# Optimization experiments

Hardware: AMD Instinct MI355X
Metric: run time of the kernel (lower is better)

## Reference

```python
import jax, jax.numpy as jnp
import numpy as np

EPS = 1e-5  # BatchNorm eps (PyTorch default)


def gcn_conv(x, edge_index, W, b):
    """PyG GCNConv with add_self_loops=True, normalize=True.
    out[j] = sum_{(i->j)} x_w[i] / sqrt(deg_i * deg_j) + x_w[j] / deg_j + b,
    deg_j = 1 + in-degree(j) (self-loop included)."""
    n = x.shape[0]
    src, dst = edge_index[0], edge_index[1]
    ones = jnp.ones(src.shape[0], x.dtype)
    deg = 1.0 + jax.ops.segment_sum(ones, dst, num_segments=n)  # [n]
    dis = jax.lax.rsqrt(deg)
    xw = x @ W  # [n, out]
    msg = xw[src] * (dis[src] * dis[dst])[:, None]  # gather + per-edge norm
    agg = jax.ops.segment_sum(msg, dst, num_segments=n)  # scatter-add
    agg = agg + xw * (1.0 / deg)[:, None]  # self-loop term
    return agg + b


def bn_relu(x, gamma, beta):
    # BatchNorm1d over the node dim (training-mode batch stats) + ReLU
    mean = x.mean(axis=0)
    var = x.var(axis=0)
    return jax.nn.relu((x - mean) * jax.lax.rsqrt(var + EPS) * gamma + beta)


def wireframe_gnn(x, edge_index, layers, fcW, fcb):
    feats = [x]
    h = x
    for (W, b, g, be) in layers:  # fixed small n_layers loop
        h = bn_relu(gcn_conv(h, edge_index, W, b), g, be)
        feats.append(h)
    cat = jnp.concatenate(feats, axis=1)
    return jax.nn.relu(cat @ fcW + fcb)


N_L, N_J = 50000, 25000
D_FC, NF = 1024, 256
E_L, E_J = 400000, 100000
L_LAB, J_LAB = 10, 3


def setup_inputs() -> dict:
    key = jax.random.key(0)
    ks = iter(jax.random.split(key, 48))
    p = lambda shape: (jax.random.normal(next(ks), shape, jnp.float32) * 0.02)
    inp = {}
    inp["line_features"] = jax.random.normal(next(ks), (N_L, D_FC), jnp.float32)
    inp["junction_features"] = jax.random.normal(next(ks), (N_J, NF), jnp.float32)
    inp["line_edge_index"] = jax.random.randint(next(ks), (2, E_L), 0, N_L, jnp.int64)
    inp["junction_edge_index"] = jax.random.randint(next(ks), (2, E_J), 0, N_J, jnp.int64)
    # line GNN: 1024 -> 512 -> 256, concat 1792 -> fc 1024
    inp["lg_W1"], inp["lg_b1"] = p((D_FC, D_FC // 2)), p((D_FC // 2,))
    inp["lg_g1"], inp["lg_be1"] = jnp.ones(D_FC // 2, jnp.float32), jnp.zeros(D_FC // 2, jnp.float32)
    inp["lg_W2"], inp["lg_b2"] = p((D_FC // 2, D_FC // 4)), p((D_FC // 4,))
    inp["lg_g2"], inp["lg_be2"] = jnp.ones(D_FC // 4, jnp.float32), jnp.zeros(D_FC // 4, jnp.float32)
    cat_l = D_FC + D_FC // 2 + D_FC // 4  # 1792
    inp["lg_fcW"], inp["lg_fcb"] = p((cat_l, D_FC)), p((D_FC,))
    # fc_lines: 1024 -> 1024 -> 1024 -> L_LAB (dim_loi*n_pts1 == dim_fc == 1024)
    inp["fl_W1"], inp["fl_b1"] = p((D_FC, D_FC)), p((D_FC,))
    inp["fl_W2"], inp["fl_b2"] = p((D_FC, D_FC)), p((D_FC,))
    inp["fl_W3"], inp["fl_b3"] = p((D_FC, L_LAB)), p((L_LAB,))
    # junction GNN: 256 -> 128 -> 64, concat 448 -> fc 256
    inp["jg_W1"], inp["jg_b1"] = p((NF, NF // 2)), p((NF // 2,))
    inp["jg_g1"], inp["jg_be1"] = jnp.ones(NF // 2, jnp.float32), jnp.zeros(NF // 2, jnp.float32)
    inp["jg_W2"], inp["jg_b2"] = p((NF // 2, NF // 4)), p((NF // 4,))
    inp["jg_g2"], inp["jg_be2"] = jnp.ones(NF // 4, jnp.float32), jnp.zeros(NF // 4, jnp.float32)
    cat_j = NF + NF // 2 + NF // 4  # 448
    inp["jg_fcW"], inp["jg_fcb"] = p((cat_j, NF)), p((NF,))
    # fc_junction: 256 -> 64 -> J_LAB
    m = NF // 4
    inp["fj_W1"], inp["fj_b1"] = p((NF, m)), p((m,))
    inp["fj_W2"], inp["fj_b2"] = p((m, J_LAB)), p((J_LAB,))
    return inp


def reference(line_features, junction_features, line_edge_index, junction_edge_index,
              lg_W1, lg_b1, lg_g1, lg_be1, lg_W2, lg_b2, lg_g2, lg_be2, lg_fcW, lg_fcb,
              fl_W1, fl_b1, fl_W2, fl_b2, fl_W3, fl_b3,
              jg_W1, jg_b1, jg_g1, jg_be1, jg_W2, jg_b2, jg_g2, jg_be2, jg_fcW, jg_fcb,
              fj_W1, fj_b1, fj_W2, fj_b2):
    # line branch
    h = wireframe_gnn(line_features, line_edge_index,
                      [(lg_W1, lg_b1, lg_g1, lg_be1), (lg_W2, lg_b2, lg_g2, lg_be2)],
                      lg_fcW, lg_fcb)
    h = jax.nn.relu(h @ fl_W1 + fl_b1)
    h = jax.nn.relu(h @ fl_W2 + fl_b2)
    line_logits = h @ fl_W3 + fl_b3
    # junction branch
    g = wireframe_gnn(junction_features, junction_edge_index,
                      [(jg_W1, jg_b1, jg_g1, jg_be1), (jg_W2, jg_b2, jg_g2, jg_be2)],
                      jg_fcW, jg_fcb)
    g = jax.nn.relu(g @ fj_W1 + fj_b1)
    junction_logits = g @ fj_W2 + fj_b2
    return (line_logits, junction_logits)
```

## Files before the change

### kernel.cpp

```cpp
#include <hip/hip_runtime.h>
#include <stdint.h>
#include <stddef.h>

typedef _Float16 f16;
typedef _Float16 f16x8 __attribute__((ext_vector_type(8)));
typedef _Float16 f16x4_t __attribute__((ext_vector_type(4)));
typedef float floatx4 __attribute__((ext_vector_type(4)));

template <int N> struct F16Vec { typedef f16 type __attribute__((ext_vector_type(N))); };

#define BN_EPS 1e-5f

struct WtJob { const float* W; f16* Wt; int K; int N; int tN; int tilebase; };
struct WtBatch { WtJob j[12]; int njobs; int ntiles; };

__global__ void k_wt_tiled(WtBatch b) {
  __shared__ float T[32][33];
  int bt = blockIdx.x;
  int i = 0;
  #pragma unroll 1
  while (i + 1 < b.njobs && bt >= b.j[i + 1].tilebase) ++i;
  WtJob J = b.j[i];
  int t = bt - J.tilebase;
  int tr = t / J.tN, tc = t - tr * J.tN;
  int ty = threadIdx.x >> 5, tx = threadIdx.x & 31;
  #pragma unroll
  for (int s = 0; s < 32; s += 8) {
    int k = tr * 32 + ty + s, n = tc * 32 + tx;
    if (k < J.K && n < J.N) T[ty + s][tx] = J.W[(size_t)k * J.N + n];
  }
  __syncthreads();
  #pragma unroll
  for (int s = 0; s < 32; s += 8) {
    int n = tc * 32 + ty + s, k = tr * 32 + tx;
    if (n < J.N && k < J.K) J.Wt[(size_t)n * J.K + k] = (f16)T[tx][ty + s];
  }
}

__global__ void k_cvt_cols(const float* __restrict__ src, f16* __restrict__ dst,
                           int n, int c, int ldd, int coff) {
  int t = blockIdx.x * blockDim.x + threadIdx.x;
  int cq = c >> 2;
  if (t >= n * cq) return;
  int r = t / cq, j = (t - r * cq) << 2;
  float4 v = *(const float4*)(src + (size_t)r * c + j);
  f16x4_t o; o[0] = (f16)v.x; o[1] = (f16)v.y; o[2] = (f16)v.z; o[3] = (f16)v.w;
  *(f16x4_t*)(dst + (size_t)r * ldd + coff + j) = o;
}

__global__ void k_count2(const int* __restrict__ dL, int EL, int* __restrict__ cntL,
                         const int* __restrict__ dJ, int EJ, int* __restrict__ cntJ) {
  int t = blockIdx.x * blockDim.x + threadIdx.x;
  if (t < EL) atomicAdd(&cntL[dL[t]], 1);
  else if (t < EL + EJ) atomicAdd(&cntJ[dJ[t - EL]], 1);
}

__global__ void k_scan4(const int* __restrict__ cnt, int n, int* __restrict__ rowstart,
                        float* __restrict__ dis) {
  __shared__ int wsum[16];
  __shared__ int carry_s;
  int tid = threadIdx.x, lane = tid & 63, wv = tid >> 6;
  if (tid == 0) { carry_s = 0; rowstart[0] = 0; }
  __syncthreads();
  for (int base = 0; base < n; base += 4096) {
    int i4 = base + tid * 4;
    int4 c = {0, 0, 0, 0};
    if (i4 < n) c = *(const int4*)(cnt + i4);
    int s0 = c.x, s1 = s0 + c.y, s2 = s1 + c.z, s3 = s2 + c.w;
    int x = s3;
    #pragma unroll
    for (int off = 1; off < 64; off <<= 1) {
      int y = __shfl_up(x, off, 64);
      if (lane >= off) x += y;
    }
    if (lane == 63) wsum[wv] = x;
    __syncthreads();
    if (wv == 0) {
      int s = (lane < 16) ? wsum[lane] : 0;
      #pragma unroll
      for (int off = 1; off < 16; off <<= 1) {
        int y = __shfl_up(s, off, 64);
        if (lane >= off) s += y;
      }
      if (lane < 16) wsum[lane] = s;
    }
    __syncthreads();
    int waveoff = (wv == 0) ? 0 : wsum[wv - 1];
    int excl = (x - s3) + waveoff + carry_s;
    if (i4 < n) {
      rowstart[i4 + 1] = excl + s0;
      rowstart[i4 + 2] = excl + s1;
      rowstart[i4 + 3] = excl + s2;
      rowstart[i4 + 4] = excl + s3;
      dis[i4 + 0] = rsqrtf(1.0f + (float)c.x);
      dis[i4 + 1] = rsqrtf(1.0f + (float)c.y);
      dis[i4 + 2] = rsqrtf(1.0f + (float)c.z);
      dis[i4 + 3] = rsqrtf(1.0f + (float)c.w);
    }
    __syncthreads();
    if (tid == 1023) carry_s = excl + s3;
    __syncthreads();
  }
}

__global__ void k_fill2(const int* __restrict__ eiL, int EL, const int* __restrict__ rsL,
                        int* __restrict__ fillL, int* __restrict__ cixL,
                        const int* __restrict__ eiJ, int EJ, const int* __restrict__ rsJ,
                        int* __restrict__ fillJ, int* __restrict__ cixJ) {
  int t = blockIdx.x * blockDim.x + threadIdx.x;
  if (t < EL) {
    int s = eiL[t], d = eiL[EL + t];
    int pos = atomicAdd(&fillL[d], 1);
    cixL[rsL[d] + pos] = s;
  } else if (t < EL + EJ) {
    int u = t - EL;
    int s = eiJ[u], d = eiJ[EJ + u];
    int pos = atomicAdd(&fillJ[d], 1);
    cixJ[rsJ[d] + pos] = s;
  }
}

template <int CPL>
__global__ void k_gather_f16(const f16* __restrict__ xw, int C,
                             const int* __restrict__ rowstart, const int* __restrict__ colidx,
                             const float* __restrict__ dis, const float* __restrict__ bias,
                             f16* __restrict__ dst, int ldd, int coff, int n) {
  typedef typename F16Vec<CPL>::type V;
  int w = threadIdx.x >> 6, l = threadIdx.x & 63;
  int j = blockIdx.x * 4 + w;
  if (j >= n) return;
  float dj = dis[j];
  int rs = rowstart[j], re = rowstart[j + 1];
  int c0 = l * CPL;
  float acc[CPL];
  {
    V p = *(const V*)(xw + (size_t)j * C + c0);
    float s = dj * dj;
    #pragma unroll
    for (int t = 0; t < CPL; ++t) acc[t] = (float)p[t] * s;
  }
  int e = rs;
  for (; e + 2 <= re; e += 2) {
    int s0 = colidx[e], s1 = colidx[e + 1];
    float f0 = dis[s0] * dj, f1 = dis[s1] * dj;
    V p0 = *(const V*)(xw + (size_t)s0 * C + c0);
    V p1 = *(const V*)(xw + (size_t)s1 * C + c0);
    #pragma unroll
    for (int t = 0; t < CPL; ++t) acc[t] += (float)p0[t] * f0 + (float)p1[t] * f1;
  }
  if (e < re) {
    int s0 = colidx[e];
    float f0 = dis[s0] * dj;
    V p0 = *(const V*)(xw + (size_t)s0 * C + c0);
    #pragma unroll
    for (int t = 0; t < CPL; ++t) acc[t] += (float)p0[t] * f0;
  }
  V o;
  #pragma unroll
  for (int t = 0; t < CPL; ++t) o[t] = (f16)(acc[t] + bias[c0 + t]);
  *(V*)(dst + (size_t)j * ldd + coff + c0) = o;
}

__global__ void k_stats(const f16* __restrict__ v, int ldd, int coff, int n, int C,
                        float* __restrict__ sum, float* __restrict__ sumsq) {
  int c = blockIdx.x * blockDim.x + threadIdx.x;
  if (c >= C) return;
  int r0 = blockIdx.y * 128, r1 = min(r0 + 128, n);
  float s = 0.f, s2 = 0.f;
  for (int r = r0; r < r1; ++r) {
    float x = (float)v[(size_t)r * ldd + coff + c];
    s += x; s2 += x * x;
  }
  atomicAdd(&sum[c], s);
  atomicAdd(&sumsq[c], s2);
}

__global__ void k_bnparam(const float* __restrict__ sum, const float* __restrict__ sumsq,
                          const float* __restrict__ gamma, const float* __restrict__ beta,
                          int n, int C, float* __restrict__ scale, float* __restrict__ shift) {
  int c = blockIdx.x * blockDim.x + threadIdx.x;
  if (c >= C) return;
  float mean = sum[c] / (float)n;
  float var = sumsq[c] / (float)n - mean * mean;
  float sc = gamma[c] * rsqrtf(var + BN_EPS);
  scale[c] = sc;
  shift[c] = beta[c] - mean * sc;
}

__global__ void k_bnapply_ip(f16* __restrict__ v, int ldd, int coff, int n, int C,
                             const float* __restrict__ scale, const float* __restrict__ shift) {
  int t = blockIdx.x * blockDim.x + threadIdx.x;
  int cq = C >> 2;
  if (t >= n * cq) return;
  int r = t / cq, c = (t - r * cq) << 2;
  f16* p = v + (size_t)r * ldd + coff + c;
  f16x4_t x = *(f16x4_t*)p;
  float4 sc = *(const float4*)(scale + c);
  float4 sh = *(const float4*)(shift + c);
  f16x4_t o;
  o[0] = (f16)fmaxf((float)x[0] * sc.x + sh.x, 0.f);
  o[1] = (f16)fmaxf((float)x[1] * sc.y + sh.y, 0.f);
  o[2] = (f16)fmaxf((float)x[2] * sc.z + sh.z, 0.f);
  o[3] = (f16)fmaxf((float)x[3] * sc.w + sh.w, 0.f);
  *(f16x4_t*)p = o;
}

__global__ __launch_bounds__(256)
void k_gemm(const f16* __restrict__ A, int lda,
            const f16* __restrict__ Bt,
            void* __restrict__ Cv, int ldc,
            const float* __restrict__ bias, int relu, int outf,
            int M, int N, int K, int mt, int nt, int per) {
  __shared__ f16 Ash[2][128 * 32];
  __shared__ f16 Bsh[2][128 * 32];
  int b = blockIdx.x;
  int g = (b & 7) * per + (b >> 3);
  if (g >= mt * nt) return;
  int tm = (g / nt) * 128, tn = (g % nt) * 128;
  int tid = threadIdx.x, l = tid & 63, w = tid >> 6;

  const f16* ag[2]; const f16* bg[2];
  uint32_t lof[2];
  #pragma unroll
  for (int j = 0; j < 2; ++j) {
    int rl = w * 32 + j * 16 + (l >> 2);
    int ck = l & 3;
    int lc = ck ^ ((rl >> 1) & 3);
    int gr = tm + rl; if (gr > M - 1) gr = M - 1;
    int gn = tn + rl; if (gn > N - 1) gn = N - 1;
    ag[j] = A + (size_t)gr * lda + lc * 8;
    bg[j] = Bt + (size_t)gn * K + lc * 8;
    lof[j] = (uint32_t)(w * 32 + j * 16) * 64;
  }

  int wm = (w >> 1) * 64, wn = (w & 1) * 64;
  int q = l >> 4, l15 = l & 15;
  uint32_t aoffb[4], boffb[4];
  #pragma unroll
  for (int i = 0; i < 4; ++i) {
    int m = wm + i * 16 + l15;
    int n2 = wn + i * 16 + l15;
    aoffb[i] = (uint32_t)(m * 32 + (q ^ ((m >> 1) & 3)) * 8) * 2;
    boffb[i] = (uint32_t)(n2 * 32 + (q ^ ((n2 >> 1) & 3)) * 8) * 2;
  }

  floatx4 acc[4][4];
  #pragma unroll
  for (int i = 0; i < 4; ++i)
    #pragma unroll
    for (int j = 0; j < 4; ++j) acc[i][j] = (floatx4){0.f, 0.f, 0.f, 0.f};

  int nk = K >> 5;
  #pragma unroll
  for (int j = 0; j < 2; ++j) {
    __builtin_amdgcn_global_load_lds(
        (const __attribute__((address_space(1))) void*)ag[j],
        (__attribute__((address_space(3))) void*)((char*)Ash + lof[j]), 16, 0, 0);
    __builtin_amdgcn_global_load_lds(
        (const __attribute__((address_space(1))) void*)bg[j],
        (__attribute__((address_space(3))) void*)((char*)Bsh + lof[j]), 16, 0, 0);
    ag[j] += 32; bg[j] += 32;
  }

  for (int i = 0; i < nk; ++i) {
    __syncthreads();
    if (i + 1 < nk) {
      uint32_t d = ((i + 1) & 1) ? 8192u : 0u;
      #pragma unroll
      for (int j = 0; j < 2; ++j) {
        __builtin_amdgcn_global_load_lds(
            (const __attribute__((address_space(1))) void*)ag[j],
            (__attribute__((address_space(3))) void*)((char*)Ash + d + lof[j]), 16, 0, 0);
        __builtin_amdgcn_global_load_lds(
            (const __attribute__((address_space(1))) void*)bg[j],
            (__attribute__((address_space(3))) void*)((char*)Bsh + d + lof[j]), 16, 0, 0);
        ag[j] += 32; bg[j] += 32;
      }
    }
    uint32_t s = (i & 1) ? 8192u : 0u;
    f16x8 af[4], bf[4];
    #pragma unroll
    for (int ii = 0; ii < 4; ++ii) {
      af[ii] = *(const f16x8*)((const char*)Ash + s + aoffb[ii]);
      bf[ii] = *(const f16x8*)((const char*)Bsh + s + boffb[ii]);
    }
    #pragma unroll
    for (int mi = 0; mi < 4; ++mi)
      #pragma unroll
      for (int ni = 0; ni < 4; ++ni)
        acc[mi][ni] = __builtin_amdgcn_mfma_f32_16x16x32_f16(af[mi], bf[ni], acc[mi][ni], 0, 0, 0);
  }

  #pragma unroll
  for (int ni = 0; ni < 4; ++ni) {
    int col = tn + wn + ni * 16 + l15;
    if (col >= N) continue;
    float bv = bias ? bias[col] : 0.f;
    #pragma unroll
    for (int mi = 0; mi < 4; ++mi) {
      int rowb = tm + wm + mi * 16 + q * 4;
      #pragma unroll
      for (int r = 0; r < 4; ++r) {
        int row = rowb + r;
        if (row < M) {
          float v = acc[mi][ni][r] + bv;
          if (relu) v = fmaxf(v, 0.f);
          if (outf) ((float*)Cv)[(size_t)row * ldc + col] = v;
          else      ((f16*)Cv)[(size_t)row * ldc + col] = (f16)v;
        }
      }
    }
  }
}

#define G_BAR()   __builtin_amdgcn_s_barrier()
#define G_LGKM0() asm volatile("s_waitcnt lgkmcnt(0)" ::: "memory")

#define MFMA_PHASE(NI, B0v, B1v)                                              \
  __builtin_amdgcn_s_setprio(1);                                              \
  _Pragma("unroll")                                                           \
  for (int mi = 0; mi < 8; ++mi) {                                            \
    acc[mi][NI] = __builtin_amdgcn_mfma_f32_16x16x32_f16(B0v, af[mi][0], acc[mi][NI], 0, 0, 0); \
    acc[mi][NI] = __builtin_amdgcn_mfma_f32_16x16x32_f16(B1v, af[mi][1], acc[mi][NI], 0, 0, 0); \
  }                                                                           \
  __builtin_amdgcn_s_setprio(0);

__global__ __launch_bounds__(512, 2)
void k_gemm256(const f16* __restrict__ A, int lda,
               const f16* __restrict__ Bt,
               f16* __restrict__ C, int ldc,
               const float* __restrict__ bias, int relu,
               int M, int N, int K, int mt, int nt) {
  __shared__ char lds[131072];
  char* ldsc = (char*)lds;
  int nwg = mt * nt;
  int b = blockIdx.x;
  int xcd = b & 7, lid = b >> 3;
  int q8 = nwg >> 3, r8 = nwg & 7;
  int wg = (xcd < r8 ? xcd * (q8 + 1) : r8 * (q8 + 1) + (xcd - r8) * q8) + lid;
  int tm = (wg / nt) * 256, tn = (wg % nt) * 256;
  int tid = threadIdx.x, l = tid & 63, w = tid >> 6;
  int wm = w >> 2, wn = w & 3;
  int q = l >> 4, l15 = l & 15;
  int nk = K >> 6;

  int r0 = tid >> 3, r1 = r0 + 64;
  int ck = (tid & 7) ^ (r0 & 7);
  int gmA0a = tm + r0;        if (gmA0a > M - 1) gmA0a = M - 1;
  int gmA0b = tm + r1;        if (gmA0b > M - 1) gmA0b = M - 1;
  int gmA1a = tm + 128 + r0;  if (gmA1a > M - 1) gmA1a = M - 1;
  int gmA1b = tm + 128 + r1;  if (gmA1b > M - 1) gmA1b = M - 1;
  int gnB0a = tn + r0;        if (gnB0a > N - 1) gnB0a = N - 1;
  int gnB0b = tn + r1;        if (gnB0b > N - 1) gnB0b = N - 1;
  int gnB1a = tn + 128 + r0;  if (gnB1a > N - 1) gnB1a = N - 1;
  int gnB1b = tn + 128 + r1;  if (gnB1b > N - 1) gnB1b = N - 1;
  const f16* pA0a = A + (size_t)gmA0a * lda + ck * 8;
  const f16* pA0b = A + (size_t)gmA0b * lda + ck * 8;
  const f16* pA1a = A + (size_t)gmA1a * lda + ck * 8;
  const f16* pA1b = A + (size_t)gmA1b * lda + ck * 8;
  const f16* pB0a = Bt + (size_t)gnB0a * K + ck * 8;
  const f16* pB0b = Bt + (size_t)gnB0b * K + ck * 8;
  const f16* pB1a = Bt + (size_t)gnB1a * K + ck * 8;
  const f16* pB1b = Bt + (size_t)gnB1b * K + ck * 8;
  uint32_t dst0 = (uint32_t)tid * 16;

  auto ST2 = [&](const f16*& pa, const f16*& pb, uint32_t dst) {
    __builtin_amdgcn_global_load_lds(
        (const __attribute__((address_space(1))) void*)pa,
        (__attribute__((address_space(3))) void*)(ldsc + dst), 16, 0, 0);
    __builtin_amdgcn_global_load_lds(
        (const __attribute__((address_space(1))) void*)pb,
        (__attribute__((address_space(3))) void*)(ldsc + dst + 8192), 16, 0, 0);
    pa += 64; pb += 64;
  };
  auto SA0 = [&](uint32_t bb) { ST2(pA0a, pA0b, bb + dst0); };
  auto SA1 = [&](uint32_t bb) { ST2(pA1a, pA1b, bb + 16384u + dst0); };
  auto SB0 = [&](uint32_t bb) { ST2(pB0a, pB0b, bb + 32768u + dst0); };
  auto SB1 = [&](uint32_t bb) { ST2(pB1a, pB1b, bb + 49152u + dst0); };

  uint32_t abase = (uint32_t)((wm * 128 + l15) * 128);
  uint32_t bbase = (uint32_t)(32768 + (wn * 64 + l15) * 128);
  uint32_t cof0 = (uint32_t)(((0 + q) ^ (l15 & 7)) * 16);
  uint32_t cof1 = (uint32_t)(((4 + q) ^ (l15 & 7)) * 16);

  floatx4 acc[8][4];
  #pragma unroll
  for (int i = 0; i < 8; ++i)
    #pragma unroll
    for (int j = 0; j < 4; ++j) acc[i][j] = (floatx4){0.f, 0.f, 0.f, 0.f};

  SA0(0u); SA1(0u); SB0(0u); SB1(0u);
  if (nk > 1) { SA0(65536u); SA1(65536u); SB0(65536u); }
  asm volatile("s_waitcnt vmcnt(6)" ::: "memory");
  G_BAR();

  f16x8 af[8][2];
  for (int t = 0; t < nk; ++t) {
    uint32_t cb = (t & 1) ? 65536u : 0u;
    uint32_t ob = 65536u - cb;
    const char* cbp = ldsc + cb;
    if (t + 1 < nk) SB1(ob);
    #pragma unroll
    for (int mi = 0; mi < 8; ++mi) {
      af[mi][0] = *(const f16x8*)(cbp + abase + mi * 2048 + cof0);
      af[mi][1] = *(const f16x8*)(cbp + abase + mi * 2048 + cof1);
    }
    f16x8 b00 = *(const f16x8*)(cbp + bbase + cof0);
    f16x8 b01 = *(const f16x8*)(cbp + bbase + cof1);
    G_BAR(); G_LGKM0();
    MFMA_PHASE(0, b00, b01);
    G_BAR();
    if (t + 2 < nk) SA0(cb);
    f16x8 b10 = *(const f16x8*)(cbp + bbase + 2048 + cof0);
    f16x8 b11 = *(const f16x8*)(cbp + bbase + 2048 + cof1);
    G_BAR(); G_LGKM0();
    MFMA_PHASE(1, b10, b11);
    G_BAR();
    if (t + 2 < nk) SA1(cb);
    f16x8 b20 = *(const f16x8*)(cbp + bbase + 4096 + cof0);
    f16x8 b21 = *(const f16x8*)(cbp + bbase + 4096 + cof1);
    f16x8 b30 = *(const f16x8*)(cbp + bbase + 6144 + cof0);
    f16x8 b31 = *(const f16x8*)(cbp + bbase + 6144 + cof1);
    G_BAR(); G_LGKM0();
    MFMA_PHASE(2, b20, b21);
    G_BAR();
    if (t + 2 < nk) {
      SB0(cb);
      asm volatile("s_waitcnt vmcnt(6)" ::: "memory");
    } else {
      asm volatile("s_waitcnt vmcnt(0)" ::: "memory");
    }
    G_BAR();
    MFMA_PHASE(3, b30, b31);
  }

  #pragma unroll
  for (int mi = 0; mi < 8; ++mi) {
    int m = tm + wm * 128 + mi * 16 + l15;
    if (m >= M) continue;
    f16* crow = C + (size_t)m * ldc;
    #pragma unroll
    for (int ni = 0; ni < 4; ++ni) {
      int n0 = tn + wn * 64 + ni * 16 + q * 4;
      floatx4 v = acc[mi][ni];
      if (bias) {
        float4 bv = *(const float4*)(bias + n0);
        v[0] += bv.x; v[1] += bv.y; v[2] += bv.z; v[3] += bv.w;
      }
      if (relu) {
        v[0] = fmaxf(v[0], 0.f); v[1] = fmaxf(v[1], 0.f);
        v[2] = fmaxf(v[2], 0.f); v[3] = fmaxf(v[3], 0.f);
      }
      f16x4_t o;
      o[0] = (f16)v[0]; o[1] = (f16)v[1]; o[2] = (f16)v[2]; o[3] = (f16)v[3];
      *(f16x4_t*)(crow + n0) = o;
    }
  }
}

extern "C" void kernel_launch(void* const* d_in, const int* in_sizes, int n_in,
                              void* d_out, int out_size, void* d_ws, size_t ws_size,
                              hipStream_t stream) {
  (void)in_sizes; (void)n_in; (void)out_size; (void)ws_size;
  const int NL = 50000, NJ = 25000, EL = 400000, EJ = 100000;

  const float* x_l  = (const float*)d_in[0];
  const float* x_j  = (const float*)d_in[1];
  const int*   ei_l = (const int*)d_in[2];
  const int*   ei_j = (const int*)d_in[3];
  const float* lgW1 = (const float*)d_in[4];  const float* lgb1 = (const float*)d_in[5];
  const float* lgg1 = (const float*)d_in[6];  const float* lgbe1= (const float*)d_in[7];
  const float* lgW2 = (const float*)d_in[8];  const float* lgb2 = (const float*)d_in[9];
  const float* lgg2 = (const float*)d_in[10]; const float* lgbe2= (const float*)d_in[11];
  const float* lgfcW= (const float*)d_in[12]; const float* lgfcb= (const float*)d_in[13];
  const float* flW1 = (const float*)d_in[14]; const float* flb1 = (const float*)d_in[15];
  const float* flW2 = (const float*)d_in[16]; const float* flb2 = (const float*)d_in[17];
  const float* flW3 = (const float*)d_in[18]; const float* flb3 = (const float*)d_in[19];
  const float* jgW1 = (const float*)d_in[20]; const float* jgb1 = (const float*)d_in[21];
  const float* jgg1 = (const float*)d_in[22]; const float* jgbe1= (const float*)d_in[23];
  const float* jgW2 = (const float*)d_in[24]; const float* jgb2 = (const float*)d_in[25];
  const float* jgg2 = (const float*)d_in[26]; const float* jgbe2= (const float*)d_in[27];
  const float* jgfcW= (const float*)d_in[28]; const float* jgfcb= (const float*)d_in[29];
  const float* fjW1 = (const float*)d_in[30]; const float* fjb1 = (const float*)d_in[31];
  const float* fjW2 = (const float*)d_in[32]; const float* fjb2 = (const float*)d_in[33];

  char* ws = (char*)d_ws;
  size_t off = 0;
  auto alloc = [&](size_t bytes) -> char* {
    char* p = ws + off;
    off += (bytes + 255) & ~(size_t)255;
    return p;
  };

  f16* cat16 = (f16*)alloc((size_t)NL * 1792 * 2);
  f16* hA    = (f16*)alloc((size_t)NL * 1024 * 2);
  f16* hB    = (f16*)alloc((size_t)NL * 1024 * 2);
  f16*  xw16  = (f16*)hB;
  f16* catJ  = (f16*)alloc((size_t)NJ * 448 * 2);
  f16* hJA   = (f16*)alloc((size_t)NJ * 256 * 2);
  f16* hJB   = (f16*)alloc((size_t)NJ * 64 * 2);
  f16*  xwJ   = (f16*)hB;

  f16* W1t   = (f16*)alloc((size_t)1024 * 512 * 2);
  f16* W2t   = (f16*)alloc((size_t)512 * 256 * 2);
  f16* fcWt  = (f16*)alloc((size_t)1792 * 1024 * 2);
  f16* flW1t = (f16*)alloc((size_t)1024 * 1024 * 2);
  f16* flW2t = (f16*)alloc((size_t)1024 * 1024 * 2);
  f16* flW3t = (f16*)alloc((size_t)1024 * 16 * 2);
  f16* jW1t  = (f16*)alloc((size_t)256 * 128 * 2);
  f16* jW2t  = (f16*)alloc((size_t)128 * 64 * 2);
  f16* jfcWt = (f16*)alloc((size_t)448 * 256 * 2);
  f16* fjW1t = (f16*)alloc((size_t)256 * 64 * 2);
  f16* fjW2t = (f16*)alloc((size_t)64 * 4 * 2);

  int* zero0 = (int*)alloc(((size_t)2 * NL + 2 * NJ + 1920) * 4);
  int* cntL  = zero0;
  int* fillL = cntL + NL;
  int* cntJ  = fillL + NL;
  int* fillJ = cntJ + NJ;
  float* stats = (float*)(fillJ + NJ);
  float* sum1L = stats;        float* sq1L = stats + 512;
  float* sum2L = stats + 1024; float* sq2L = stats + 1280;
  float* sum1J = stats + 1536; float* sq1J = stats + 1664;
  float* sum2J = stats + 1792; float* sq2J = stats + 1856;

  int* rsL   = (int*)alloc((size_t)(NL + 4) * 4);
  int* cixL  = (int*)alloc((size_t)EL * 4);
  float* disL= (float*)alloc((size_t)NL * 4);
  int* rsJ   = (int*)alloc((size_t)(NJ + 4) * 4);
  int* cixJ  = (int*)alloc((size_t)EJ * 4);
  float* disJ= (float*)alloc((size_t)NJ * 4);
  float* scalc = (float*)alloc(512 * 4);
  float* shftc = (float*)alloc(512 * 4);

  auto cdiv = [](int a, int b) { return (a + b - 1) / b; };

  auto gemm = [&](const f16* A, int lda, const f16* Bt, void* Cc, int ldc,
                  const float* bias, int relu, int outf, int M, int N, int K) {
    if (!outf && (N & 255) == 0 && N >= 256 && (K & 63) == 0 && K >= 128) {
      int mt = cdiv(M, 256), nt = N >> 8;
      k_gemm256<<<mt * nt, 512, 0, stream>>>(A, lda, Bt, (f16*)Cc, ldc, bias, relu,
                                             M, N, K, mt, nt);
    } else {
      int mt = cdiv(M, 128), nt = cdiv(N, 128);
      int per = cdiv(mt * nt, 8);
      k_gemm<<<8 * per, 256, 0, stream>>>(A, lda, Bt, Cc, ldc, bias, relu, outf,
                                          M, N, K, mt, nt, per);
    }
  };
  auto bn = [&](f16* v, int ldd, int coff, int n, int C,
                float* sum, float* sumsq, const float* gamma, const float* beta) {
    dim3 gs(cdiv(C, 256), cdiv(n, 128));
    k_stats<<<gs, 256, 0, stream>>>(v, ldd, coff, n, C, sum, sumsq);
    k_bnparam<<<cdiv(C, 256), 256, 0, stream>>>(sum, sumsq, gamma, beta, n, C, scalc, shftc);
    k_bnapply_ip<<<cdiv(n * (C >> 2), 256), 256, 0, stream>>>(v, ldd, coff, n, C, scalc, shftc);
  };

  hipMemsetAsync(zero0, 0, ((size_t)2 * NL + 2 * NJ + 1920) * 4, stream);

  {
    WtBatch B2; int base = 0, nj = 0;
    auto add = [&](const float* W, f16* Wt, int K, int N) {
      int tK = cdiv(K, 32), tN = cdiv(N, 32);
      B2.j[nj++] = WtJob{W, Wt, K, N, tN, base};
      base += tK * tN;
    };
    add(lgW1, W1t, 1024, 512);
    add(lgW2, W2t, 512, 256);
    add(lgfcW, fcWt, 1792, 1024);
    add(flW1, flW1t, 1024, 1024);
    add(flW2, flW2t, 1024, 1024);
    add(flW3, flW3t, 1024, 10);
    add(jgW1, jW1t, 256, 128);
    add(jgW2, jW2t, 128, 64);
    add(jgfcW, jfcWt, 448, 256);
    add(fjW1, fjW1t, 256, 64);
    add(fjW2, fjW2t, 64, 3);
    B2.njobs = nj; B2.ntiles = base;
    k_wt_tiled<<<base, 256, 0, stream>>>(B2);
  }

  k_cvt_cols<<<cdiv(NL * 256, 256), 256, 0, stream>>>(x_l, cat16, NL, 1024, 1792, 0);
  k_cvt_cols<<<cdiv(NJ * 64, 256), 256, 0, stream>>>(x_j, catJ, NJ, 256, 448, 0);

  k_count2<<<cdiv(EL + EJ, 256), 256, 0, stream>>>(ei_l + EL, EL, cntL, ei_j + EJ, EJ, cntJ);
  k_scan4<<<1, 1024, 0, stream>>>(cntL, NL, rsL, disL);
  k_scan4<<<1, 1024, 0, stream>>>(cntJ, NJ, rsJ, disJ);
  k_fill2<<<cdiv(EL + EJ, 256), 256, 0, stream>>>(ei_l, EL, rsL, fillL, cixL,
                                                  ei_j, EJ, rsJ, fillJ, cixJ);

  gemm(cat16, 1792, W1t, xw16, 512, nullptr, 0, 0, NL, 512, 1024);
  k_gather_f16<8><<<cdiv(NL, 4), 256, 0, stream>>>(xw16, 512, rsL, cixL, disL, lgb1,
                                                   cat16, 1792, 1024, NL);
  bn(cat16, 1792, 1024, NL, 512, sum1L, sq1L, lgg1, lgbe1);

  gemm(cat16 + 1024, 1792, W2t, xw16, 256, nullptr, 0, 0, NL, 256, 512);
  k_gather_f16<4><<<cdiv(NL, 4), 256, 0, stream>>>(xw16, 256, rsL, cixL, disL, lgb2,
                                                   cat16, 1792, 1536, NL);
  bn(cat16, 1792, 1536, NL, 256, sum2L, sq2L, lgg2, lgbe2);

  gemm(cat16, 1792, fcWt, hA, 1024, lgfcb, 1, 0, NL, 1024, 1792);
  gemm(hA, 1024, flW1t, hB, 1024, flb1, 1, 0, NL, 1024, 1024);
  gemm(hB, 1024, flW2t, hA, 1024, flb2, 1, 0, NL, 1024, 1024);
  gemm(hA, 1024, flW3t, (float*)d_out, 10, flb3, 0, 1, NL, 10, 1024);

  gemm(catJ, 448, jW1t, xwJ, 128, nullptr, 0, 0, NJ, 128, 256);
  k_gather_f16<2><<<cdiv(NJ, 4), 256, 0, stream>>>(xwJ, 128, rsJ, cixJ, disJ, jgb1,
                                                   catJ, 448, 256, NJ);
  bn(catJ, 448, 256, NJ, 128, sum1J, sq1J, jgg1, jgbe1);

  gemm(catJ + 256, 448, jW2t, xwJ, 64, nullptr, 0, 0, NJ, 64, 128);
  k_gather_f16<1><<<cdiv(NJ, 4), 256, 0, stream>>>(xwJ, 64, rsJ, cixJ, disJ, jgb2,
                                                   catJ, 448, 384, NJ);
  bn(catJ, 448, 384, NJ, 64, sum2J, sq2J, jgg2, jgbe2);

  gemm(catJ, 448, jfcWt, hJA, 256, jgfcb, 1, 0, NJ, 256, 448);
  gemm(hJA, 256, fjW1t, hJB, 64, fjb1, 1, 0, NJ, 64, 256);
  gemm(hJB, 64, fjW2t, (float*)d_out + (size_t)NL * 10, 3, fjb2, 0, 1, NJ, 3, 64);
}
```

Before: 1.507 ms.

## Restructure 256x256 GEMM main loop to stream A fragments per M-pair

```diff
diff --git a/kernel.cpp b/kernel.cpp
--- a/kernel.cpp
+++ b/kernel.cpp
@@ -313,15 +313,30 @@
   }
 }
 
-#define G_BAR()   __builtin_amdgcn_s_barrier()
+#define G_BAR()   asm volatile("s_barrier" ::: "memory")
 #define G_LGKM0() asm volatile("s_waitcnt lgkmcnt(0)" ::: "memory")
 
-#define MFMA_PHASE(NI, B0v, B1v)                                              \
+#define READ_BF_ALL()                                                         \
+  _Pragma("unroll")                                                           \
+  for (int ni = 0; ni < 4; ++ni) {                                            \
+    bf[ni][0] = *(const f16x8*)(cbp + bbase + ni * 2048 + cof0);              \
+    bf[ni][1] = *(const f16x8*)(cbp + bbase + ni * 2048 + cof1);              \
+  }
+
+#define READ_AFP(P)                                                           \
+  afp[0][0] = *(const f16x8*)(cbp + abase + (2 * (P)) * 2048 + cof0);         \
+  afp[0][1] = *(const f16x8*)(cbp + abase + (2 * (P)) * 2048 + cof1);         \
+  afp[1][0] = *(const f16x8*)(cbp + abase + (2 * (P) + 1) * 2048 + cof0);     \
+  afp[1][1] = *(const f16x8*)(cbp + abase + (2 * (P) + 1) * 2048 + cof1);
+
+#define MFMA_PAIR(P)                                                          \
   __builtin_amdgcn_s_setprio(1);                                              \
   _Pragma("unroll")                                                           \
-  for (int mi = 0; mi < 8; ++mi) {                                            \
-    acc[mi][NI] = __builtin_amdgcn_mfma_f32_16x16x32_f16(B0v, af[mi][0], acc[mi][NI], 0, 0, 0); \
-    acc[mi][NI] = __builtin_amdgcn_mfma_f32_16x16x32_f16(B1v, af[mi][1], acc[mi][NI], 0, 0, 0); \
+  for (int ni = 0; ni < 4; ++ni) {                                            \
+    acc[2*(P)][ni]   = __builtin_amdgcn_mfma_f32_16x16x32_f16(bf[ni][0], afp[0][0], acc[2*(P)][ni], 0, 0, 0);   \
+    acc[2*(P)][ni]   = __builtin_amdgcn_mfma_f32_16x16x32_f16(bf[ni][1], afp[0][1], acc[2*(P)][ni], 0, 0, 0);   \
+    acc[2*(P)+1][ni] = __builtin_amdgcn_mfma_f32_16x16x32_f16(bf[ni][0], afp[1][0], acc[2*(P)+1][ni], 0, 0, 0); \
+    acc[2*(P)+1][ni] = __builtin_amdgcn_mfma_f32_16x16x32_f16(bf[ni][1], afp[1][1], acc[2*(P)+1][ni], 0, 0, 0); \
   }                                                                           \
   __builtin_amdgcn_s_setprio(0);
 
@@ -390,48 +405,36 @@
     for (int j = 0; j < 4; ++j) acc[i][j] = (floatx4){0.f, 0.f, 0.f, 0.f};
 
   SA0(0u); SA1(0u); SB0(0u); SB1(0u);
-  if (nk > 1) { SA0(65536u); SA1(65536u); SB0(65536u); }
-  asm volatile("s_waitcnt vmcnt(6)" ::: "memory");
-  G_BAR();
-
-  f16x8 af[8][2];
+  if (nk > 1) { SB0(65536u); SB1(65536u); }
+
+  f16x8 bf[4][2], afp[2][2];
   for (int t = 0; t < nk; ++t) {
     uint32_t cb = (t & 1) ? 65536u : 0u;
     uint32_t ob = 65536u - cb;
     const char* cbp = ldsc + cb;
-    if (t + 1 < nk) SB1(ob);
-    #pragma unroll
-    for (int mi = 0; mi < 8; ++mi) {
-      af[mi][0] = *(const f16x8*)(cbp + abase + mi * 2048 + cof0);
-      af[mi][1] = *(const f16x8*)(cbp + abase + mi * 2048 + cof1);
-    }
-    f16x8 b00 = *(const f16x8*)(cbp + bbase + cof0);
-    f16x8 b01 = *(const f16x8*)(cbp + bbase + cof1);
-    G_BAR(); G_LGKM0();
-    MFMA_PHASE(0, b00, b01);
+    if (t + 1 < nk) { asm volatile("s_waitcnt vmcnt(4)" ::: "memory"); }
+    else            { asm volatile("s_waitcnt vmcnt(0)" ::: "memory"); }
     G_BAR();
-    if (t + 2 < nk) SA0(cb);
-    f16x8 b10 = *(const f16x8*)(cbp + bbase + 2048 + cof0);
-    f16x8 b11 = *(const f16x8*)(cbp + bbase + 2048 + cof1);
-    G_BAR(); G_LGKM0();
-    MFMA_PHASE(1, b10, b11);
+    if (t + 1 < nk) SA0(ob);
+    READ_BF_ALL();
+    READ_AFP(0);
+    G_LGKM0();
+    MFMA_PAIR(0);
     G_BAR();
-    if (t + 2 < nk) SA1(cb);
-    f16x8 b20 = *(const f16x8*)(cbp + bbase + 4096 + cof0);
-    f16x8 b21 = *(const f16x8*)(cbp + bbase + 4096 + cof1);
-    f16x8 b30 = *(const f16x8*)(cbp + bbase + 6144 + cof0);
-    f16x8 b31 = *(const f16x8*)(cbp + bbase + 6144 + cof1);
-    G_BAR(); G_LGKM0();
-    MFMA_PHASE(2, b20, b21);
+    if (t + 1 < nk) SA1(ob);
+    READ_AFP(1);
+    G_LGKM0();
+    MFMA_PAIR(1);
     G_BAR();
-    if (t + 2 < nk) {
-      SB0(cb);
-      asm volatile("s_waitcnt vmcnt(6)" ::: "memory");
-    } else {
-      asm volatile("s_waitcnt vmcnt(0)" ::: "memory");
-    }
+    if (t + 2 < nk) SB0(cb);
+    READ_AFP(2);
+    G_LGKM0();
+    MFMA_PAIR(2);
     G_BAR();
-    MFMA_PHASE(3, b30, b31);
+    if (t + 2 < nk) SB1(cb);
+    READ_AFP(3);
+    G_LGKM0();
+    MFMA_PAIR(3);
   }
 
   #pragma unroll
```

Result: no change. 1.506 ms (-0.0%).
